# Kernel optimization log

Measured on AMD Instinct MI355X. Metric: run time of the kernel, lower is better.

The kernel has to match this reference:

```python
import jax, jax.numpy as jnp
import numpy as np

HEADS = 4
DIM_HEAD = 64
SCALE = 10.0
EPS = 1e-12  # matches torch F.normalize default eps


def setup_inputs() -> dict:
    key = jax.random.key(0)
    k1, k2, k3, k4, k5 = jax.random.split(key, 5)
    dim = 256
    hidden = HEADS * DIM_HEAD
    x = jax.random.normal(k1, (16, dim, 32, 32), dtype=jnp.float32)
    y = jax.random.normal(k2, (16, dim, 32, 32), dtype=jnp.float32)
    # 1x1 conv weights stored as 2D matrices (out_ch, in_ch)
    w_qkv = jax.random.normal(k3, (hidden * 3, dim), dtype=jnp.float32) * (1.0 / np.sqrt(dim))
    w_out = jax.random.normal(k4, (dim, hidden), dtype=jnp.float32) * (1.0 / np.sqrt(hidden))
    b_out = jax.random.normal(k5, (dim,), dtype=jnp.float32) * 0.01
    return {"x": x, "y": y, "w_qkv": w_qkv, "w_out": w_out, "b_out": b_out}


def _l2norm(t):
    # torch F.normalize(t, dim=-1): t / max(||t||_2, eps)
    n = jnp.sqrt(jnp.sum(t * t, axis=-1, keepdims=True))
    return t / jnp.maximum(n, EPS)


def reference(x, y, w_qkv, w_out, b_out):
    b, c, hh, ww = x.shape
    n_x = hh * ww
    n_y = y.shape[2] * y.shape[3]
    hidden = HEADS * DIM_HEAD

    # 1x1 convs == channel matmuls; only q from x and k,v from y are used
    w_q, w_k, w_v = w_qkv[:hidden], w_qkv[hidden:2 * hidden], w_qkv[2 * hidden:]
    q = jnp.einsum('oc,bcn->bon', w_q, x.reshape(b, c, n_x)).reshape(b, HEADS, DIM_HEAD, n_x)
    k = jnp.einsum('oc,bcn->bon', w_k, y.reshape(b, c, n_y)).reshape(b, HEADS, DIM_HEAD, n_y)
    v = jnp.einsum('oc,bcn->bon', w_v, y.reshape(b, c, n_y)).reshape(b, HEADS, DIM_HEAD, n_y)

    # l2norm over the spatial (last) axis, as in the source
    q = _l2norm(q)
    k = _l2norm(k)

    sim = jnp.einsum('bhdi,bhdj->bhij', q, k) * SCALE          # [b,h,n_x,n_y]
    attn = jax.nn.softmax(sim, axis=-1)
    out = jnp.einsum('bhij,bhdj->bhid', attn, v)                # [b,h,n_x,d]

    # 'b h (x y) d -> b (h d) x y'
    out = out.transpose(0, 1, 3, 2).reshape(b, hidden, hh, ww)
    out = jnp.einsum('oc,bcn->bon', w_out, out.reshape(b, hidden, n_x))
    out = out + b_out[None, :, None]
    return out.reshape(b, -1, hh, ww)
```

## Files before the change

kernel.cpp:

```cpp
#include <hip/hip_runtime.h>
#include <hip/hip_bf16.h>
#include <stdint.h>

typedef __attribute__((ext_vector_type(8))) short short8;
typedef __attribute__((ext_vector_type(4))) float f32x4;
typedef __attribute__((ext_vector_type(4))) unsigned short ushort4v;

#define MFMA16(a, b, c) __builtin_amdgcn_mfma_f32_16x16x32_bf16((a), (b), (c), 0, 0, 0)


__device__ __forceinline__ ushort f2bf(float f) {
  union { float f; unsigned u; } x; x.f = f;
  unsigned r = x.u + 0x7FFFu + ((x.u >> 16) & 1u);
  return (ushort)(r >> 16);
}

__device__ __forceinline__ short8 ld8(const ushort* p) {
  return *reinterpret_cast<const short8*>(p);
}

__device__ __forceinline__ void gll16(const void* g, void* l) {
  __builtin_amdgcn_global_load_lds(
      reinterpret_cast<const __attribute__((address_space(1))) unsigned int*>(
          reinterpret_cast<uintptr_t>(g)),
      reinterpret_cast<__attribute__((address_space(3))) unsigned int*>(
          reinterpret_cast<uintptr_t>(l)),
      16, 0, 0);
}

__device__ __forceinline__ void stage_tile(const char* gbase, char* ldsbase,
                                           int goff, int ldsw) {
#pragma unroll
  for (int c = 0; c < 8; ++c)
    gll16(gbase + c * 8192 + goff, ldsbase + c * 8192 + ldsw);
}

__global__ __launch_bounds__(256) void k_tcvt(const float* __restrict__ x,
    const float* __restrict__ y, ushort* __restrict__ xbt, ushort* __restrict__ ybt,
    const float* __restrict__ wqkv, const float* __restrict__ wout,
    ushort* __restrict__ wqkvb, ushort* __restrict__ woutb) {
  int tile = blockIdx.x;
  if (tile >= 2048) {
    const int total1 = 768 * 256;
    const int total = total1 + 256 * 256;
    for (int i = (tile - 2048) * 256 + threadIdx.x; i < total; i += 64 * 256) {
      if (i < total1) wqkvb[i] = f2bf(wqkv[i]);
      else woutb[i - total1] = f2bf(wout[i - total1]);
    }
    return;
  }
  const float* src; ushort* dst;
  if (tile >= 1024) { tile -= 1024; src = y; dst = ybt; }
  else { src = x; dst = xbt; }
  int b = tile >> 6;
  int c0 = ((tile >> 4) & 3) << 6;
  int n0 = (tile & 15) << 6;
  __shared__ ushort lds[64][65];
  int tid = threadIdx.x;
  int nl = tid & 63, cl = tid >> 6;
  const float* sb = src + ((size_t)b << 18);
#pragma unroll
  for (int s = 0; s < 16; ++s) {
    int c = cl + (s << 2);
    lds[c][nl] = f2bf(sb[(size_t)(c0 + c) * 1024 + n0 + nl]);
  }
  __syncthreads();
  ushort* db = dst + ((size_t)b << 18);
  int cl2 = tid & 63, nl2 = tid >> 6;
#pragma unroll
  for (int s = 0; s < 16; ++s) {
    int n = nl2 + (s << 2);
    db[(size_t)(n0 + n) * 256 + c0 + cl2] = lds[cl2][n];
  }
}

__global__ __launch_bounds__(512, 2) void k_qkv(const ushort* __restrict__ wqkvb,
    const ushort* __restrict__ xbt, const ushort* __restrict__ ybt,
    ushort* __restrict__ qt, ushort* __restrict__ kt, ushort* __restrict__ vbuf) {
  int bid = blockIdx.x;
  int lid = (bid & 7) * 48 + (bid >> 3);
  int ox = lid % 24;
  int b = lid / 24;
  int o0 = ox * 32;
  const ushort* Bsrc = (o0 < 256) ? xbt : ybt;
  const char* Bm = (const char*)(Bsrc + ((size_t)b << 18));
  int tid = threadIdx.x;
  int l = tid & 63, w = tid >> 6;
  int r = l & 15, g = l >> 4;

  __shared__ __align__(16) char Bt[2][65536];
  __shared__ float snorm[8][32];
  __shared__ float fs[32];

  const ushort* Ab = wqkvb + (size_t)(o0 + r) * 256 + g * 8;
  short8 areg[2][8];
#pragma unroll
  for (int ks = 0; ks < 8; ++ks) {
    areg[0][ks] = ld8(Ab + ks * 32);
    areg[1][ks] = ld8(Ab + 4096 + ks * 32);
  }

  int Lb = tid * 16;
  int trow = Lb >> 9;
  int goff = trow * 512 + ((Lb & 511) ^ ((trow & 7) << 4));
  int ldsw = w * 1024;

  f32x4 acc[2][8];
#pragma unroll
  for (int i = 0; i < 2; ++i)
#pragma unroll
    for (int j = 0; j < 8; ++j) acc[i][j] = (f32x4){0.f, 0.f, 0.f, 0.f};

  stage_tile(Bm, &Bt[0][0], goff, ldsw);
  __syncthreads();

  int rr = w * 16 + r;
  int sw = (r & 7) << 4;
  for (int nt = 0; nt < 8; ++nt) {
    int cur = nt & 1;
    if (nt < 7) stage_tile(Bm + (size_t)(nt + 1) * 65536, &Bt[cur ^ 1][0], goff, ldsw);
    const char* Bc = &Bt[cur][0];
#pragma unroll
    for (int ks = 0; ks < 8; ++ks) {
      short8 bv = *reinterpret_cast<const short8*>(Bc + rr * 512 + ((ks * 64 + g * 16) ^ sw));
      acc[0][nt] = MFMA16(areg[0][ks], bv, acc[0][nt]);
      acc[1][nt] = MFMA16(areg[1][ks], bv, acc[1][nt]);
    }
    __syncthreads();
  }

  if (o0 < 512) {
    float ss[2][4];
#pragma unroll
    for (int mf = 0; mf < 2; ++mf)
#pragma unroll
      for (int reg = 0; reg < 4; ++reg) {
        float s = 0.f;
#pragma unroll
        for (int nt = 0; nt < 8; ++nt) { float v = acc[mf][nt][reg]; s += v * v; }
#pragma unroll
        for (int m = 1; m < 16; m <<= 1) s += __shfl_xor(s, m);
        ss[mf][reg] = s;
      }
    if (r == 0) {
#pragma unroll
      for (int mf = 0; mf < 2; ++mf)
#pragma unroll
        for (int reg = 0; reg < 4; ++reg)
          snorm[w][mf * 16 + g * 4 + reg] = ss[mf][reg];
    }
    __syncthreads();
    if (tid < 32) {
      float s = 0.f;
#pragma unroll
      for (int w2 = 0; w2 < 8; ++w2) s += snorm[w2][tid];
      fs[tid] = ((o0 < 256) ? 10.0f : 1.0f) / fmaxf(sqrtf(s), 1e-12f);
    }
    __syncthreads();
    float fr[2][4];
#pragma unroll
    for (int mf = 0; mf < 2; ++mf)
#pragma unroll
      for (int reg = 0; reg < 4; ++reg) fr[mf][reg] = fs[mf * 16 + g * 4 + reg];
    int od = (o0 < 256) ? o0 : o0 - 256;
    int hh = od >> 6, d0 = od & 63;
    ushort* dst = ((o0 < 256) ? qt : kt) + (((size_t)(b * 4 + hh)) << 16);
#pragma unroll
    for (int mf = 0; mf < 2; ++mf)
#pragma unroll
      for (int nt = 0; nt < 8; ++nt) {
        int n = nt * 128 + w * 16 + r;
        ushort4v u;
#pragma unroll
        for (int reg = 0; reg < 4; ++reg) u[reg] = f2bf(acc[mf][nt][reg] * fr[mf][reg]);
        *reinterpret_cast<ushort4v*>(dst + (size_t)n * 64 + d0 + mf * 16 + g * 4) = u;
      }
  } else {
#pragma unroll
    for (int mf = 0; mf < 2; ++mf) {
      int ob = o0 - 512 + mf * 16 + g * 4;
#pragma unroll
      for (int nt = 0; nt < 8; ++nt) {
        int n = nt * 128 + w * 16 + r;
#pragma unroll
        for (int reg = 0; reg < 4; ++reg)
          vbuf[(((size_t)b * 256 + ob + reg) << 10) + n] = f2bf(acc[mf][nt][reg]);
      }
    }
  }
}

__global__ __launch_bounds__(512, 4) void k_attn(const ushort* __restrict__ qt,
    const ushort* __restrict__ kt, const ushort* __restrict__ vbuf,
    ushort* __restrict__ aot) {
  int hb = blockIdx.x;
  int it = blockIdx.y;
  int h = hb & 3, b = hb >> 2;
  int tid = threadIdx.x;
  int l = tid & 63, w = tid >> 6;
  int r = l & 15, g = l >> 4;
  size_t ho = ((size_t)hb) << 16;
  const ushort* Q = qt + ho;
  const char* Kg = (const char*)(kt + ho);
  const char* Vg = (const char*)(vbuf + ((size_t)b << 18) + ((size_t)h << 16));
  int i0 = it * 128 + w * 16;

  __shared__ __align__(16) ushort Kb[2][4096];
  __shared__ __align__(16) ushort Vb[2][4096];
  __shared__ __align__(16) ushort plds[8][1024];

  int L = w * 1024 + l * 16;
  int srow = L >> 7;
  int swz = (srow & 7) << 4;
  int ksrc = L ^ swz;
  int vsrc_col = (L & 127) ^ swz;

  short8 qa[2];
#pragma unroll
  for (int ks = 0; ks < 2; ++ks)
    qa[ks] = ld8(Q + (size_t)(i0 + r) * 64 + ks * 32 + g * 8);

  f32x4 oacc[4];
  float rsum[4];
#pragma unroll
  for (int j = 0; j < 4; ++j) { oacc[j] = (f32x4){0.f, 0.f, 0.f, 0.f}; rsum[j] = 0.f; }

#define STAGE(buf, j0v) do { \
    gll16(Kg + (j0v) * 128 + ksrc, (char*)&Kb[buf][0] + w * 1024); \
    gll16(Vg + (size_t)srow * 2048 + (j0v) * 2 + vsrc_col, (char*)&Vb[buf][0] + w * 1024); \
  } while (0)

  STAGE(0, 0);
  __syncthreads();

  char* plc = (char*)plds[w];
  for (int t = 0; t < 16; ++t) {
    int cur = t & 1;
    if (t < 15) STAGE(cur ^ 1, (t + 1) * 64);
    const char* Kc = (const char*)&Kb[cur][0];
    const char* Vc = (const char*)&Vb[cur][0];
    f32x4 sacc[4];
#pragma unroll
    for (int nf = 0; nf < 4; ++nf) sacc[nf] = (f32x4){0.f, 0.f, 0.f, 0.f};
#pragma unroll
    for (int nf = 0; nf < 4; ++nf) {
      int row = nf * 16 + r;
      int sw = (row & 7) << 4;
      short8 k0 = *reinterpret_cast<const short8*>(Kc + ((row * 128 + g * 16) ^ sw));
      short8 k1 = *reinterpret_cast<const short8*>(Kc + ((row * 128 + 64 + g * 16) ^ sw));
      sacc[nf] = MFMA16(qa[0], k0, sacc[nf]);
      sacc[nf] = MFMA16(qa[1], k1, sacc[nf]);
    }
#pragma unroll
    for (int nf = 0; nf < 4; ++nf)
#pragma unroll
      for (int reg = 0; reg < 4; ++reg) {
        float p = __expf(sacc[nf][reg]);
        rsum[reg] += p;
        union { float f; unsigned u; } cv; cv.f = p;
        int row = g * 4 + reg;
        int xorv = ((row ^ (row >> 3)) & 7) << 4;
        int byteo = row * 128 + (((nf * 16 + r) * 2) ^ xorv);
        *(ushort*)(plc + byteo) = (ushort)(cv.u >> 16);
      }
    short8 pa[2];
#pragma unroll
    for (int ks = 0; ks < 2; ++ks) {
      int xorv = (r ^ (r >> 3)) & 7;
      int blk = (ks * 4 + g) ^ xorv;
      pa[ks] = *reinterpret_cast<const short8*>(plc + r * 128 + blk * 16);
    }
#pragma unroll
    for (int df = 0; df < 4; ++df) {
      int row = df * 16 + r;
      int sw = (row & 7) << 4;
#pragma unroll
      for (int ks = 0; ks < 2; ++ks) {
        short8 vf = *reinterpret_cast<const short8*>(Vc + ((row * 128 + ks * 64 + g * 16) ^ sw));
        oacc[df] = MFMA16(pa[ks], vf, oacc[df]);
      }
    }
    __syncthreads();
  }
#undef STAGE

#pragma unroll
  for (int reg = 0; reg < 4; ++reg) {
    float s = rsum[reg];
#pragma unroll
    for (int m = 1; m < 16; m <<= 1) s += __shfl_xor(s, m);
    rsum[reg] = 1.0f / s;
  }
#pragma unroll
  for (int df = 0; df < 4; ++df)
#pragma unroll
    for (int reg = 0; reg < 4; ++reg) {
      int i = i0 + g * 4 + reg;
      int d = df * 16 + r;
      float vo = oacc[df][reg] * rsum[reg];
      aot[((size_t)b << 18) + (size_t)i * 256 + h * 64 + d] = f2bf(vo);
    }
}

__global__ __launch_bounds__(512, 2) void k_out(const ushort* __restrict__ woutb,
    const ushort* __restrict__ aot, const float* __restrict__ bout,
    float* __restrict__ out) {
  int bid = blockIdx.x;
  int lid = (bid & 7) * 32 + (bid >> 3);
  int ox = lid & 7;
  int t = lid >> 3;
  int nb = t & 1;
  int b = t >> 1;
  int o0 = ox * 32;
  int tid = threadIdx.x, l = tid & 63, w = tid >> 6, r = l & 15, g = l >> 4;
  const char* Bm = (const char*)(aot + ((size_t)b << 18) + ((size_t)nb << 17));

  __shared__ __align__(16) char Bt[2][65536];

  const ushort* Ab = woutb + (size_t)(o0 + r) * 256 + g * 8;
  short8 areg[2][8];
#pragma unroll
  for (int ks = 0; ks < 8; ++ks) {
    areg[0][ks] = ld8(Ab + ks * 32);
    areg[1][ks] = ld8(Ab + 4096 + ks * 32);
  }

  int Lb = tid * 16;
  int trow = Lb >> 9;
  int goff = trow * 512 + ((Lb & 511) ^ ((trow & 7) << 4));
  int ldsw = w * 1024;

  f32x4 acc[2][4];
#pragma unroll
  for (int i = 0; i < 2; ++i)
#pragma unroll
    for (int j = 0; j < 4; ++j) acc[i][j] = (f32x4){0.f, 0.f, 0.f, 0.f};

  stage_tile(Bm, &Bt[0][0], goff, ldsw);
  __syncthreads();

  int rr = w * 16 + r;
  int sw = (r & 7) << 4;
  for (int nt = 0; nt < 4; ++nt) {
    int cur = nt & 1;
    if (nt < 3) stage_tile(Bm + (size_t)(nt + 1) * 65536, &Bt[cur ^ 1][0], goff, ldsw);
    const char* Bc = &Bt[cur][0];
#pragma unroll
    for (int ks = 0; ks < 8; ++ks) {
      short8 bv = *reinterpret_cast<const short8*>(Bc + rr * 512 + ((ks * 64 + g * 16) ^ sw));
      acc[0][nt] = MFMA16(areg[0][ks], bv, acc[0][nt]);
      acc[1][nt] = MFMA16(areg[1][ks], bv, acc[1][nt]);
    }
    __syncthreads();
  }

  float bias[2][4];
#pragma unroll
  for (int mf = 0; mf < 2; ++mf)
#pragma unroll
    for (int reg = 0; reg < 4; ++reg) bias[mf][reg] = bout[o0 + mf * 16 + g * 4 + reg];
#pragma unroll
  for (int mf = 0; mf < 2; ++mf)
#pragma unroll
    for (int nt = 0; nt < 4; ++nt)
#pragma unroll
      for (int reg = 0; reg < 4; ++reg) {
        size_t o = (size_t)(b * 256 + o0 + mf * 16 + g * 4 + reg);
        int n = nb * 512 + nt * 128 + w * 16 + r;
        out[(o << 10) + n] = acc[mf][nt][reg] + bias[mf][reg];
      }
}

extern "C" void kernel_launch(void* const* d_in, const int* in_sizes, int n_in,
                              void* d_out, int out_size, void* d_ws, size_t ws_size,
                              hipStream_t stream) {
  const float* x     = (const float*)d_in[0];
  const float* y     = (const float*)d_in[1];
  const float* wqkv  = (const float*)d_in[2];
  const float* wout  = (const float*)d_in[3];
  const float* bout  = (const float*)d_in[4];
  float* out = (float*)d_out;
  char* ws = (char*)d_ws;

  ushort* xbt   = (ushort*)(ws + 0ull);
  ushort* aot   = (ushort*)(ws + 0ull);
  ushort* ybt   = (ushort*)(ws + 8388608ull);
  ushort* qt    = (ushort*)(ws + 16777216ull);
  ushort* kt    = (ushort*)(ws + 25165824ull);
  ushort* vbuf  = (ushort*)(ws + 33554432ull);
  ushort* wqkvb = (ushort*)(ws + 41943040ull);
  ushort* woutb = (ushort*)(ws + 42336256ull);

  k_tcvt<<<2112, 256, 0, stream>>>(x, y, xbt, ybt, wqkv, wout, wqkvb, woutb);
  k_qkv<<<384, 512, 0, stream>>>(wqkvb, xbt, ybt, qt, kt, vbuf);
  k_attn<<<dim3(64, 8), 512, 0, stream>>>(qt, kt, vbuf, aot);
  k_out<<<256, 512, 0, stream>>>(woutb, aot, bout, out);
}
```

Baseline: 160.8 us.

## Halve GEMM LDS tiles, stream weights from global, vectorize transpose-convert kernel

```diff
diff --git a/kernel.cpp b/kernel.cpp
--- a/kernel.cpp
+++ b/kernel.cpp
@@ -28,11 +28,11 @@
       16, 0, 0);
 }
 
-__device__ __forceinline__ void stage_tile(const char* gbase, char* ldsbase,
-                                           int goff, int ldsw) {
-#pragma unroll
-  for (int c = 0; c < 8; ++c)
-    gll16(gbase + c * 8192 + goff, ldsbase + c * 8192 + ldsw);
+__device__ __forceinline__ void stage_tile32(const char* gbase, char* ldsbase,
+                                             int goff, int ldsw) {
+#pragma unroll
+  for (int c = 0; c < 4; ++c)
+    gll16(gbase + c * 16384 + goff, ldsbase + c * 8192 + ldsw);
 }
 
 __global__ __launch_bounds__(256) void k_tcvt(const float* __restrict__ x,
@@ -41,11 +41,19 @@
     ushort* __restrict__ wqkvb, ushort* __restrict__ woutb) {
   int tile = blockIdx.x;
   if (tile >= 2048) {
-    const int total1 = 768 * 256;
-    const int total = total1 + 256 * 256;
-    for (int i = (tile - 2048) * 256 + threadIdx.x; i < total; i += 64 * 256) {
-      if (i < total1) wqkvb[i] = f2bf(wqkv[i]);
-      else woutb[i - total1] = f2bf(wout[i - total1]);
+    const int t1 = 49152;
+    const int tot = t1 + 16384;
+    for (int i = (tile - 2048) * 256 + threadIdx.x; i < tot; i += 64 * 256) {
+      if (i < t1) {
+        float4 v = reinterpret_cast<const float4*>(wqkv)[i];
+        ushort4v u = {f2bf(v.x), f2bf(v.y), f2bf(v.z), f2bf(v.w)};
+        reinterpret_cast<ushort4v*>(wqkvb)[i] = u;
+      } else {
+        int j = i - t1;
+        float4 v = reinterpret_cast<const float4*>(wout)[j];
+        ushort4v u = {f2bf(v.x), f2bf(v.y), f2bf(v.z), f2bf(v.w)};
+        reinterpret_cast<ushort4v*>(woutb)[j] = u;
+      }
     }
     return;
   }
@@ -55,26 +63,31 @@
   int b = tile >> 6;
   int c0 = ((tile >> 4) & 3) << 6;
   int n0 = (tile & 15) << 6;
-  __shared__ ushort lds[64][65];
+  __shared__ ushort ldsT[64][72];
   int tid = threadIdx.x;
-  int nl = tid & 63, cl = tid >> 6;
   const float* sb = src + ((size_t)b << 18);
-#pragma unroll
-  for (int s = 0; s < 16; ++s) {
-    int c = cl + (s << 2);
-    lds[c][nl] = f2bf(sb[(size_t)(c0 + c) * 1024 + n0 + nl]);
+  int cc = tid >> 4, n4 = tid & 15;
+#pragma unroll
+  for (int s = 0; s < 4; ++s) {
+    int c = cc + s * 16;
+    float4 v = *reinterpret_cast<const float4*>(sb + (size_t)(c0 + c) * 1024 + n0 + n4 * 4);
+    ldsT[n4 * 4 + 0][c] = f2bf(v.x);
+    ldsT[n4 * 4 + 1][c] = f2bf(v.y);
+    ldsT[n4 * 4 + 2][c] = f2bf(v.z);
+    ldsT[n4 * 4 + 3][c] = f2bf(v.w);
   }
   __syncthreads();
   ushort* db = dst + ((size_t)b << 18);
-  int cl2 = tid & 63, nl2 = tid >> 6;
-#pragma unroll
-  for (int s = 0; s < 16; ++s) {
-    int n = nl2 + (s << 2);
-    db[(size_t)(n0 + n) * 256 + c0 + cl2] = lds[cl2][n];
-  }
-}
-
-__global__ __launch_bounds__(512, 2) void k_qkv(const ushort* __restrict__ wqkvb,
+  int nn = tid >> 4, c4 = tid & 15;
+#pragma unroll
+  for (int s = 0; s < 4; ++s) {
+    int n = nn + s * 16;
+    ushort4v u = *reinterpret_cast<const ushort4v*>(&ldsT[n][c4 * 4]);
+    *reinterpret_cast<ushort4v*>(db + (size_t)(n0 + n) * 256 + c0 + c4 * 4) = u;
+  }
+}
+
+__global__ __launch_bounds__(512, 4) void k_qkv(const ushort* __restrict__ wqkvb,
     const ushort* __restrict__ xbt, const ushort* __restrict__ ybt,
     ushort* __restrict__ qt, ushort* __restrict__ kt, ushort* __restrict__ vbuf) {
   int bid = blockIdx.x;
@@ -88,21 +101,15 @@
   int l = tid & 63, w = tid >> 6;
   int r = l & 15, g = l >> 4;
 
-  __shared__ __align__(16) char Bt[2][65536];
+  __shared__ __align__(16) char Bt[2][32768];
   __shared__ float snorm[8][32];
   __shared__ float fs[32];
 
   const ushort* Ab = wqkvb + (size_t)(o0 + r) * 256 + g * 8;
-  short8 areg[2][8];
-#pragma unroll
-  for (int ks = 0; ks < 8; ++ks) {
-    areg[0][ks] = ld8(Ab + ks * 32);
-    areg[1][ks] = ld8(Ab + 4096 + ks * 32);
-  }
 
   int Lb = tid * 16;
-  int trow = Lb >> 9;
-  int goff = trow * 512 + ((Lb & 511) ^ ((trow & 7) << 4));
+  int trow = Lb >> 8;
+  int goff = trow * 512 + ((Lb & 255) ^ ((trow & 7) << 4));
   int ldsw = w * 1024;
 
   f32x4 acc[2][8];
@@ -111,20 +118,28 @@
 #pragma unroll
     for (int j = 0; j < 8; ++j) acc[i][j] = (f32x4){0.f, 0.f, 0.f, 0.f};
 
-  stage_tile(Bm, &Bt[0][0], goff, ldsw);
+  stage_tile32(Bm, &Bt[0][0], goff, ldsw);
   __syncthreads();
 
   int rr = w * 16 + r;
   int sw = (r & 7) << 4;
-  for (int nt = 0; nt < 8; ++nt) {
-    int cur = nt & 1;
-    if (nt < 7) stage_tile(Bm + (size_t)(nt + 1) * 65536, &Bt[cur ^ 1][0], goff, ldsw);
+  for (int t = 0; t < 16; ++t) {
+    int cur = t & 1;
+    if (t < 15) {
+      int t1 = t + 1;
+      stage_tile32(Bm + (size_t)(t1 >> 1) * 65536 + (t1 & 1) * 256,
+                   &Bt[cur ^ 1][0], goff, ldsw);
+    }
     const char* Bc = &Bt[cur][0];
-#pragma unroll
-    for (int ks = 0; ks < 8; ++ks) {
-      short8 bv = *reinterpret_cast<const short8*>(Bc + rr * 512 + ((ks * 64 + g * 16) ^ sw));
-      acc[0][nt] = MFMA16(areg[0][ks], bv, acc[0][nt]);
-      acc[1][nt] = MFMA16(areg[1][ks], bv, acc[1][nt]);
+    int nchunk = t >> 1, chalf = t & 1;
+#pragma unroll
+    for (int ks4 = 0; ks4 < 4; ++ks4) {
+      int ks = chalf * 4 + ks4;
+      short8 a0 = ld8(Ab + ks * 32);
+      short8 a1 = ld8(Ab + 4096 + ks * 32);
+      short8 bv = *reinterpret_cast<const short8*>(Bc + rr * 256 + ((ks4 * 64 + g * 16) ^ sw));
+      acc[0][nchunk] = MFMA16(a0, bv, acc[0][nchunk]);
+      acc[1][nchunk] = MFMA16(a1, bv, acc[1][nchunk]);
     }
     __syncthreads();
   }
@@ -302,54 +317,56 @@
     }
 }
 
-__global__ __launch_bounds__(512, 2) void k_out(const ushort* __restrict__ woutb,
+__global__ __launch_bounds__(512, 4) void k_out(const ushort* __restrict__ woutb,
     const ushort* __restrict__ aot, const float* __restrict__ bout,
     float* __restrict__ out) {
   int bid = blockIdx.x;
-  int lid = (bid & 7) * 32 + (bid >> 3);
+  int lid = (bid & 7) * 64 + (bid >> 3);
   int ox = lid & 7;
-  int t = lid >> 3;
-  int nb = t & 1;
-  int b = t >> 1;
+  int t2 = lid >> 3;
+  int nq = t2 & 3;
+  int b = t2 >> 2;
   int o0 = ox * 32;
   int tid = threadIdx.x, l = tid & 63, w = tid >> 6, r = l & 15, g = l >> 4;
-  const char* Bm = (const char*)(aot + ((size_t)b << 18) + ((size_t)nb << 17));
-
-  __shared__ __align__(16) char Bt[2][65536];
+  const char* Bm = (const char*)(aot + ((size_t)b << 18) + ((size_t)nq << 16));
+
+  __shared__ __align__(16) char Bt[2][32768];
 
   const ushort* Ab = woutb + (size_t)(o0 + r) * 256 + g * 8;
-  short8 areg[2][8];
-#pragma unroll
-  for (int ks = 0; ks < 8; ++ks) {
-    areg[0][ks] = ld8(Ab + ks * 32);
-    areg[1][ks] = ld8(Ab + 4096 + ks * 32);
-  }
 
   int Lb = tid * 16;
-  int trow = Lb >> 9;
-  int goff = trow * 512 + ((Lb & 511) ^ ((trow & 7) << 4));
+  int trow = Lb >> 8;
+  int goff = trow * 512 + ((Lb & 255) ^ ((trow & 7) << 4));
   int ldsw = w * 1024;
 
-  f32x4 acc[2][4];
+  f32x4 acc[2][2];
 #pragma unroll
   for (int i = 0; i < 2; ++i)
 #pragma unroll
-    for (int j = 0; j < 4; ++j) acc[i][j] = (f32x4){0.f, 0.f, 0.f, 0.f};
-
-  stage_tile(Bm, &Bt[0][0], goff, ldsw);
+    for (int j = 0; j < 2; ++j) acc[i][j] = (f32x4){0.f, 0.f, 0.f, 0.f};
+
+  stage_tile32(Bm, &Bt[0][0], goff, ldsw);
   __syncthreads();
 
   int rr = w * 16 + r;
   int sw = (r & 7) << 4;
-  for (int nt = 0; nt < 4; ++nt) {
-    int cur = nt & 1;
-    if (nt < 3) stage_tile(Bm + (size_t)(nt + 1) * 65536, &Bt[cur ^ 1][0], goff, ldsw);
+  for (int t = 0; t < 4; ++t) {
+    int cur = t & 1;
+    if (t < 3) {
+      int t1 = t + 1;
+      stage_tile32(Bm + (size_t)(t1 >> 1) * 65536 + (t1 & 1) * 256,
+                   &Bt[cur ^ 1][0], goff, ldsw);
+    }
     const char* Bc = &Bt[cur][0];
-#pragma unroll
-    for (int ks = 0; ks < 8; ++ks) {
-      short8 bv = *reinterpret_cast<const short8*>(Bc + rr * 512 + ((ks * 64 + g * 16) ^ sw));
-      acc[0][nt] = MFMA16(areg[0][ks], bv, acc[0][nt]);
-      acc[1][nt] = MFMA16(areg[1][ks], bv, acc[1][nt]);
+    int nchunk = t >> 1, chalf = t & 1;
+#pragma unroll
+    for (int ks4 = 0; ks4 < 4; ++ks4) {
+      int ks = chalf * 4 + ks4;
+      short8 a0 = ld8(Ab + ks * 32);
+      short8 a1 = ld8(Ab + 4096 + ks * 32);
+      short8 bv = *reinterpret_cast<const short8*>(Bc + rr * 256 + ((ks4 * 64 + g * 16) ^ sw));
+      acc[0][nchunk] = MFMA16(a0, bv, acc[0][nchunk]);
+      acc[1][nchunk] = MFMA16(a1, bv, acc[1][nchunk]);
     }
     __syncthreads();
   }
@@ -362,11 +379,11 @@
 #pragma unroll
   for (int mf = 0; mf < 2; ++mf)
 #pragma unroll
-    for (int nt = 0; nt < 4; ++nt)
+    for (int nt = 0; nt < 2; ++nt)
 #pragma unroll
       for (int reg = 0; reg < 4; ++reg) {
         size_t o = (size_t)(b * 256 + o0 + mf * 16 + g * 4 + reg);
-        int n = nb * 512 + nt * 128 + w * 16 + r;
+        int n = nq * 256 + nt * 128 + w * 16 + r;
         out[(o << 10) + n] = acc[mf][nt][reg] + bias[mf][reg];
       }
 }
@@ -394,5 +411,5 @@
   k_tcvt<<<2112, 256, 0, stream>>>(x, y, xbt, ybt, wqkv, wout, wqkvb, woutb);
   k_qkv<<<384, 512, 0, stream>>>(wqkvb, xbt, ybt, qt, kt, vbuf);
   k_attn<<<dim3(64, 8), 512, 0, stream>>>(qt, kt, vbuf, aot);
-  k_out<<<256, 512, 0, stream>>>(woutb, aot, bout, out);
-}
+  k_out<<<512, 512, 0, stream>>>(woutb, aot, bout, out);
+}
```

New measurement: 185.1 us. 1.15x slower.

## Vectorize transpose-convert kernel and overlap tile prefetch with partial vmcnt waits

Applied to the files above, without the earlier changes.

```diff
diff --git a/kernel.cpp b/kernel.cpp
--- a/kernel.cpp
+++ b/kernel.cpp
@@ -41,11 +41,19 @@
     ushort* __restrict__ wqkvb, ushort* __restrict__ woutb) {
   int tile = blockIdx.x;
   if (tile >= 2048) {
-    const int total1 = 768 * 256;
-    const int total = total1 + 256 * 256;
-    for (int i = (tile - 2048) * 256 + threadIdx.x; i < total; i += 64 * 256) {
-      if (i < total1) wqkvb[i] = f2bf(wqkv[i]);
-      else woutb[i - total1] = f2bf(wout[i - total1]);
+    const int t1 = 49152;
+    const int tot = t1 + 16384;
+    for (int i = (tile - 2048) * 256 + threadIdx.x; i < tot; i += 64 * 256) {
+      if (i < t1) {
+        float4 v = reinterpret_cast<const float4*>(wqkv)[i];
+        ushort4v u = {f2bf(v.x), f2bf(v.y), f2bf(v.z), f2bf(v.w)};
+        reinterpret_cast<ushort4v*>(wqkvb)[i] = u;
+      } else {
+        int j = i - t1;
+        float4 v = reinterpret_cast<const float4*>(wout)[j];
+        ushort4v u = {f2bf(v.x), f2bf(v.y), f2bf(v.z), f2bf(v.w)};
+        reinterpret_cast<ushort4v*>(woutb)[j] = u;
+      }
     }
     return;
   }
@@ -55,22 +63,27 @@
   int b = tile >> 6;
   int c0 = ((tile >> 4) & 3) << 6;
   int n0 = (tile & 15) << 6;
-  __shared__ ushort lds[64][65];
+  __shared__ ushort ldsT[64][72];
   int tid = threadIdx.x;
-  int nl = tid & 63, cl = tid >> 6;
   const float* sb = src + ((size_t)b << 18);
-#pragma unroll
-  for (int s = 0; s < 16; ++s) {
-    int c = cl + (s << 2);
-    lds[c][nl] = f2bf(sb[(size_t)(c0 + c) * 1024 + n0 + nl]);
+  int cc = tid >> 4, n4 = tid & 15;
+#pragma unroll
+  for (int s = 0; s < 4; ++s) {
+    int c = cc + s * 16;
+    float4 v = *reinterpret_cast<const float4*>(sb + (size_t)(c0 + c) * 1024 + n0 + n4 * 4);
+    ldsT[n4 * 4 + 0][c] = f2bf(v.x);
+    ldsT[n4 * 4 + 1][c] = f2bf(v.y);
+    ldsT[n4 * 4 + 2][c] = f2bf(v.z);
+    ldsT[n4 * 4 + 3][c] = f2bf(v.w);
   }
   __syncthreads();
   ushort* db = dst + ((size_t)b << 18);
-  int cl2 = tid & 63, nl2 = tid >> 6;
-#pragma unroll
-  for (int s = 0; s < 16; ++s) {
-    int n = nl2 + (s << 2);
-    db[(size_t)(n0 + n) * 256 + c0 + cl2] = lds[cl2][n];
+  int nn = tid >> 4, c4 = tid & 15;
+#pragma unroll
+  for (int s = 0; s < 4; ++s) {
+    int n = nn + s * 16;
+    ushort4v u = *reinterpret_cast<const ushort4v*>(&ldsT[n][c4 * 4]);
+    *reinterpret_cast<ushort4v*>(db + (size_t)(n0 + n) * 256 + c0 + c4 * 4) = u;
   }
 }
 
@@ -112,13 +125,19 @@
     for (int j = 0; j < 8; ++j) acc[i][j] = (f32x4){0.f, 0.f, 0.f, 0.f};
 
   stage_tile(Bm, &Bt[0][0], goff, ldsw);
-  __syncthreads();
 
   int rr = w * 16 + r;
   int sw = (r & 7) << 4;
   for (int nt = 0; nt < 8; ++nt) {
     int cur = nt & 1;
-    if (nt < 7) stage_tile(Bm + (size_t)(nt + 1) * 65536, &Bt[cur ^ 1][0], goff, ldsw);
+    if (nt < 7) {
+      stage_tile(Bm + (size_t)(nt + 1) * 65536, &Bt[cur ^ 1][0], goff, ldsw);
+      asm volatile("s_waitcnt vmcnt(8)" ::: "memory");
+    } else {
+      asm volatile("s_waitcnt vmcnt(0)" ::: "memory");
+    }
+    __builtin_amdgcn_sched_barrier(0);
+    __builtin_amdgcn_s_barrier();
     const char* Bc = &Bt[cur][0];
 #pragma unroll
     for (int ks = 0; ks < 8; ++ks) {
@@ -126,7 +145,9 @@
       acc[0][nt] = MFMA16(areg[0][ks], bv, acc[0][nt]);
       acc[1][nt] = MFMA16(areg[1][ks], bv, acc[1][nt]);
     }
-    __syncthreads();
+    asm volatile("s_waitcnt lgkmcnt(0)" ::: "memory");
+    __builtin_amdgcn_sched_barrier(0);
+    __builtin_amdgcn_s_barrier();
   }
 
   if (o0 < 512) {
@@ -308,9 +329,9 @@
   int bid = blockIdx.x;
   int lid = (bid & 7) * 32 + (bid >> 3);
   int ox = lid & 7;
-  int t = lid >> 3;
-  int nb = t & 1;
-  int b = t >> 1;
+  int t2 = lid >> 3;
+  int nb = t2 & 1;
+  int b = t2 >> 1;
   int o0 = ox * 32;
   int tid = threadIdx.x, l = tid & 63, w = tid >> 6, r = l & 15, g = l >> 4;
   const char* Bm = (const char*)(aot + ((size_t)b << 18) + ((size_t)nb << 17));
@@ -337,13 +358,19 @@
     for (int j = 0; j < 4; ++j) acc[i][j] = (f32x4){0.f, 0.f, 0.f, 0.f};
 
   stage_tile(Bm, &Bt[0][0], goff, ldsw);
-  __syncthreads();
 
   int rr = w * 16 + r;
   int sw = (r & 7) << 4;
   for (int nt = 0; nt < 4; ++nt) {
     int cur = nt & 1;
-    if (nt < 3) stage_tile(Bm + (size_t)(nt + 1) * 65536, &Bt[cur ^ 1][0], goff, ldsw);
+    if (nt < 3) {
+      stage_tile(Bm + (size_t)(nt + 1) * 65536, &Bt[cur ^ 1][0], goff, ldsw);
+      asm volatile("s_waitcnt vmcnt(8)" ::: "memory");
+    } else {
+      asm volatile("s_waitcnt vmcnt(0)" ::: "memory");
+    }
+    __builtin_amdgcn_sched_barrier(0);
+    __builtin_amdgcn_s_barrier();
     const char* Bc = &Bt[cur][0];
 #pragma unroll
     for (int ks = 0; ks < 8; ++ks) {
@@ -351,7 +378,9 @@
       acc[0][nt] = MFMA16(areg[0][ks], bv, acc[0][nt]);
       acc[1][nt] = MFMA16(areg[1][ks], bv, acc[1][nt]);
     }
-    __syncthreads();
+    asm volatile("s_waitcnt lgkmcnt(0)" ::: "memory");
+    __builtin_amdgcn_sched_barrier(0);
+    __builtin_amdgcn_s_barrier();
   }
 
   float bias[2][4];
```

After: 157.1 us. -2.3%, faster.
